# Performance work log

Hardware: AMD Instinct MI355X
Metric: run time of the kernel (lower is better)

## Reference

```python
import jax, jax.numpy as jnp
import numpy as np


def setup_inputs() -> dict:
    key = jax.random.key(0)
    k1, k2 = jax.random.split(key)
    B, C, H, W = 32, 64, 64, 64
    K = 512
    z_e = jax.random.normal(k1, (B, C, H, W), dtype=jnp.float32)
    # codebook initialized uniform(-1/K, 1/K) as in the torch module
    codebook = jax.random.uniform(k2, (K, C), dtype=jnp.float32,
                                  minval=-1.0 / K, maxval=1.0 / K)
    return {"z_e": z_e, "codebook": codebook}


def reference(z_e, codebook):
    B, C, H, W = z_e.shape
    commitment_cost = 0.25
    # [B*H*W, C]
    z_flat = jnp.transpose(z_e, (0, 2, 3, 1)).reshape(-1, C)
    dists = (jnp.sum(z_flat * z_flat, axis=1, keepdims=True)
             + jnp.sum(codebook * codebook, axis=1)
             - 2.0 * jnp.matmul(z_flat, codebook.T))
    encoding_indices = jnp.argmin(dists, axis=1)  # [N] int
    z_q = codebook[encoding_indices].reshape(B, H, W, C)
    z_q = jnp.transpose(z_q, (0, 3, 1, 2))  # [B, C, H, W]
    q_loss = jnp.mean((z_q - jax.lax.stop_gradient(z_e)) ** 2)
    e_loss = jnp.mean((z_e - jax.lax.stop_gradient(z_q)) ** 2)
    loss = q_loss + commitment_cost * e_loss
    # straight-through estimator
    z_q_st = z_e + jax.lax.stop_gradient(z_q - z_e)
    return (z_q_st, encoding_indices, loss)
```

## Files before the change

### kernel.cpp

```cpp
#include <hip/hip_runtime.h>
#include <cfloat>

typedef __attribute__((ext_vector_type(8))) short short8;
typedef __attribute__((ext_vector_type(4))) float f32x4;

constexpr int C_DIM    = 64;
constexpr int K_CODES  = 512;
constexpr int HW       = 4096;
constexpr int CHW      = 262144;
constexpr int NPTS     = 131072;
constexpr int ZQ_SIZE  = 8388608;
constexpr int IDX_OFF  = ZQ_SIZE;
constexpr int LOSS_OFF = ZQ_SIZE + NPTS;
constexpr int TILE     = 128;
constexpr int EH_STRIDE = 72;
constexpr int CHUNK    = 128;
constexpr int NSLOT    = 16;
constexpr size_t WS_BF16 = (size_t)K_CODES * C_DIM * 2;
constexpr size_t WS_NEED = WS_BF16 + (size_t)K_CODES * 4;

__device__ __forceinline__ unsigned short f32_to_bf16_rne(float f) {
    unsigned u = __float_as_uint(f);
    unsigned r = u + 0x7fffu + ((u >> 16) & 1u);
    return (unsigned short)(r >> 16);
}

template <int STRIDE>
__device__ __forceinline__ float np_sumsq64(const float* __restrict__ a) {
    float r[8];
#pragma unroll
    for (int j = 0; j < 8; ++j) { const float v = a[j * STRIDE]; r[j] = __fmul_rn(v, v); }
#pragma unroll
    for (int i = 8; i < 64; i += 8)
#pragma unroll
        for (int j = 0; j < 8; ++j) {
            const float v = a[(i + j) * STRIDE];
            r[j] = __fadd_rn(r[j], __fmul_rn(v, v));
        }
    return __fadd_rn(
        __fadd_rn(__fadd_rn(r[0], r[1]), __fadd_rn(r[2], r[3])),
        __fadd_rn(__fadd_rn(r[4], r[5]), __fadd_rn(r[6], r[7])));
}

__global__ void vq_zero(float* __restrict__ out) { out[LOSS_OFF] = 0.0f; }

__global__ void vq_prep(const float* __restrict__ cb, unsigned short* __restrict__ wsb,
                        float* __restrict__ wsB, float* __restrict__ out) {
    const int gid = blockIdx.x * 256 + threadIdx.x;
    wsb[gid] = f32_to_bf16_rne(cb[gid]);
    if (gid < K_CODES) wsB[gid] = np_sumsq64<1>(cb + gid * C_DIM);
    if (gid == 0) out[LOSS_OFF] = 0.0f;
}

__global__ __launch_bounds__(256, 4) void vq_idx(const float* __restrict__ ze,
                                                 const float* __restrict__ cb,
                                                 float* __restrict__ out,
                                                 const unsigned short* __restrict__ wsb,
                                                 const float* __restrict__ wsB,
                                                 int use_ws)
{
    __shared__ unsigned short eh[CHUNK * EH_STRIDE];
    __shared__ float  BsL[K_CODES];
    __shared__ float  As[TILE];
    __shared__ unsigned short cand[TILE * NSLOT];
    __shared__ int    cnt[TILE];
    __shared__ int    bestk[TILE];
    __shared__ double lred[4];

    const int tid  = threadIdx.x;
    const int lane = tid & 63, w = tid >> 6;
    const int quad = lane >> 4, l15 = lane & 15;
    const int n0   = blockIdx.x * TILE;
    const int b    = n0 >> 12, hw0 = n0 & (HW - 1);
    const float* zebase = ze + b * CHW + hw0;

    if (use_ws) { for (int k = tid; k < K_CODES; k += 256) BsL[k] = wsB[k]; }
    else        { for (int k = tid; k < K_CODES; k += 256) BsL[k] = np_sumsq64<1>(cb + k * C_DIM); }
    if (tid < TILE) { As[tid] = np_sumsq64<HW>(zebase + tid); cnt[tid] = 0; }
    __syncthreads();

    short8 afr[2][2];
    float  A_pt[2][4], thr[2][4], runmin[2][4];
#pragma unroll
    for (int rt = 0; rt < 2; ++rt) {
        const int pt = w * 32 + rt * 16 + l15;
#pragma unroll
        for (int kc = 0; kc < 2; ++kc) {
            union { unsigned short s[8]; short8 v; } u;
#pragma unroll
            for (int j = 0; j < 8; ++j) {
                const int c = kc * 32 + quad * 8 + j;
                u.s[j] = f32_to_bf16_rne(zebase[c * HW + pt]);
            }
            afr[rt][kc] = u.v;
        }
#pragma unroll
        for (int r = 0; r < 4; ++r) {
            A_pt[rt][r]   = As[w * 32 + rt * 16 + quad * 4 + r];
            runmin[rt][r] = FLT_MAX;
        }
    }

    auto stage = [&](int ch) {
        const int row = tid >> 1, half = tid & 1;
        uint4* dst = (uint4*)(eh + row * EH_STRIDE + half * 32);
        if (use_ws) {
            const uint4* src = (const uint4*)(wsb + (size_t)(ch * CHUNK + row) * C_DIM + half * 32);
#pragma unroll
            for (int i = 0; i < 4; ++i) dst[i] = src[i];
        } else {
            const float4* src = (const float4*)(cb + (size_t)(ch * CHUNK + row) * C_DIM + half * 32);
#pragma unroll
            for (int i = 0; i < 4; ++i) {
                const float4 f0 = src[2 * i], f1 = src[2 * i + 1];
                uint4 o;
                o.x = (unsigned)f32_to_bf16_rne(f0.x) | ((unsigned)f32_to_bf16_rne(f0.y) << 16);
                o.y = (unsigned)f32_to_bf16_rne(f0.z) | ((unsigned)f32_to_bf16_rne(f0.w) << 16);
                o.z = (unsigned)f32_to_bf16_rne(f1.x) | ((unsigned)f32_to_bf16_rne(f1.y) << 16);
                o.w = (unsigned)f32_to_bf16_rne(f1.z) | ((unsigned)f32_to_bf16_rne(f1.w) << 16);
                dst[i] = o;
            }
        }
    };

    for (int ch = 0; ch < 4; ++ch) {
        __syncthreads(); stage(ch); __syncthreads();
        for (int tile = 0; tile < 8; ++tile) {
            const int cl = tile * 16 + l15;
            const short8 b0 = *(const short8*)(eh + cl * EH_STRIDE + quad * 8);
            const short8 b1 = *(const short8*)(eh + cl * EH_STRIDE + 32 + quad * 8);
            const float bs = BsL[ch * CHUNK + cl];
#pragma unroll
            for (int rt = 0; rt < 2; ++rt) {
                f32x4 acc = {0.f, 0.f, 0.f, 0.f};
                acc = __builtin_amdgcn_mfma_f32_16x16x32_bf16(afr[rt][0], b0, acc, 0, 0, 0);
                acc = __builtin_amdgcn_mfma_f32_16x16x32_bf16(afr[rt][1], b1, acc, 0, 0, 0);
#pragma unroll
                for (int r = 0; r < 4; ++r) {
                    const float D = fmaf(-2.f, acc[r], __fadd_rn(A_pt[rt][r], bs));
                    runmin[rt][r] = fminf(runmin[rt][r], D);
                }
            }
        }
    }
#pragma unroll
    for (int rt = 0; rt < 2; ++rt)
#pragma unroll
        for (int r = 0; r < 4; ++r) {
            float v = runmin[rt][r];
#pragma unroll
            for (int m = 1; m < 16; m <<= 1) v = fminf(v, __shfl_xor(v, m, 64));
            thr[rt][r] = v + (4e-4f * sqrtf(A_pt[rt][r]) + 3e-4f);
        }

    for (int ch = 0; ch < 4; ++ch) {
        __syncthreads(); stage(ch); __syncthreads();
        for (int tile = 0; tile < 8; ++tile) {
            const int cl = tile * 16 + l15;
            const short8 b0 = *(const short8*)(eh + cl * EH_STRIDE + quad * 8);
            const short8 b1 = *(const short8*)(eh + cl * EH_STRIDE + 32 + quad * 8);
            const float bs = BsL[ch * CHUNK + cl];
#pragma unroll
            for (int rt = 0; rt < 2; ++rt) {
                f32x4 acc = {0.f, 0.f, 0.f, 0.f};
                acc = __builtin_amdgcn_mfma_f32_16x16x32_bf16(afr[rt][0], b0, acc, 0, 0, 0);
                acc = __builtin_amdgcn_mfma_f32_16x16x32_bf16(afr[rt][1], b1, acc, 0, 0, 0);
#pragma unroll
                for (int r = 0; r < 4; ++r) {
                    const float D = fmaf(-2.f, acc[r], __fadd_rn(A_pt[rt][r], bs));
                    if (D <= thr[rt][r]) {
                        const int pt = w * 32 + rt * 16 + quad * 4 + r;
                        const int p = atomicAdd(&cnt[pt], 1);
                        if (p < NSLOT) cand[pt * NSLOT + p] = (unsigned short)(ch * CHUNK + cl);
                    }
                }
            }
        }
    }
    __syncthreads();

    if (tid < TILE) {
        const float Av = As[tid];
        const int c = cnt[tid];
        float bD = FLT_MAX; int bK = K_CODES;
        if (c <= NSLOT) {
            for (int i = 0; i < c; ++i) {
                const int k = cand[tid * NSLOT + i];
                const float* er = cb + k * C_DIM;
                float M = 0.f;
#pragma unroll
                for (int cc = 0; cc < 64; ++cc) M = fmaf(zebase[cc * HW + tid], er[cc], M);
                const float D = fmaf(-2.f, M, __fadd_rn(Av, BsL[k]));
                if (D < bD || (D == bD && k < bK)) { bD = D; bK = k; }
            }
        } else {
            for (int k = 0; k < K_CODES; ++k) {
                const float* er = cb + k * C_DIM;
                float M = 0.f;
#pragma unroll
                for (int cc = 0; cc < 64; ++cc) M = fmaf(zebase[cc * HW + tid], er[cc], M);
                const float D = fmaf(-2.f, M, __fadd_rn(Av, BsL[k]));
                if (D < bD) { bD = D; bK = k; }
            }
        }
        bestk[tid] = bK;
        out[IDX_OFF + n0 + tid] = (float)bK;
    }
    __syncthreads();

    double ls = 0.0;
#pragma unroll
    for (int it = 0; it < 8; ++it) {
        const int task = tid + 256 * it;
        const int c = task >> 5, q = task & 31;
        const float4 xz = *(const float4*)(zebase + c * HW + 4 * q);
        float o[4];
#pragma unroll
        for (int j = 0; j < 4; ++j) {
            const int k = bestk[4 * q + j];
            const float ev = cb[k * C_DIM + c];
            const float xv = (j == 0) ? xz.x : (j == 1) ? xz.y : (j == 2) ? xz.z : xz.w;
            const float d = __fsub_rn(ev, xv);
            o[j] = __fadd_rn(xv, d);
            ls = fma((double)d, (double)d, ls);
        }
        *(float4*)(out + b * CHW + c * HW + hw0 + 4 * q) = make_float4(o[0], o[1], o[2], o[3]);
    }
#pragma unroll
    for (int off = 32; off > 0; off >>= 1) ls += __shfl_xor(ls, off, 64);
    if ((tid & 63) == 0) lred[w] = ls;
    __syncthreads();
    if (tid == 0)
        atomicAdd(out + LOSS_OFF,
                  (float)((lred[0] + lred[1] + lred[2] + lred[3]) * (1.25 / (double)ZQ_SIZE)));
}

extern "C" void kernel_launch(void* const* d_in, const int* in_sizes, int n_in,
                              void* d_out, int out_size, void* d_ws, size_t ws_size,
                              hipStream_t stream) {
    (void)in_sizes; (void)n_in; (void)out_size;
    const float* ze = (const float*)d_in[0];
    const float* cb = (const float*)d_in[1];
    float* out = (float*)d_out;
    const int use_ws = (ws_size >= WS_NEED) ? 1 : 0;
    unsigned short* wsb = (unsigned short*)d_ws;
    float* wsB = (float*)((char*)d_ws + WS_BF16);

    if (use_ws) vq_prep<<<(K_CODES * C_DIM) / 256, 256, 0, stream>>>(cb, wsb, wsB, out);
    else        vq_zero<<<1, 1, 0, stream>>>(out);
    vq_idx<<<NPTS / TILE, 256, 0, stream>>>(ze, cb, out, wsb, wsB, use_ws);
}
```

Baseline: 140.9 us.

## Fuse two-pass candidate search into single pass with per-lane top-2 tracking

Replaces the separate min pass and threshold-filter pass over the codebook with one MFMA pass that keeps each lane's best two scores and a third-best sentinel, then builds candidate lists from those after a cross-lane min reduction. This halves the MFMA and LDS staging work, and staging now uses 256-code chunks with an XOR-swizzled unpadded LDS layout. Per-point norm computation and fp32 refinement are split across thread pairs so all 256 threads work. The trade-offs are higher register use for the top-2 state and a tighter threshold. Any lane whose third-best falls inside the threshold forces the full fp32 fallback scan.

Measured after the change: 355.5 us. 2.52x slower.

```diff
diff --git a/kernel.cpp b/kernel.cpp
--- a/kernel.cpp
+++ b/kernel.cpp
@@ -13,9 +13,8 @@
 constexpr int IDX_OFF  = ZQ_SIZE;
 constexpr int LOSS_OFF = ZQ_SIZE + NPTS;
 constexpr int TILE     = 128;
-constexpr int EH_STRIDE = 72;
-constexpr int CHUNK    = 128;
-constexpr int NSLOT    = 16;
+constexpr int CHUNK    = 256;
+constexpr int NSLOT    = 8;
 constexpr size_t WS_BF16 = (size_t)K_CODES * C_DIM * 2;
 constexpr size_t WS_NEED = WS_BF16 + (size_t)K_CODES * 4;
 
@@ -40,6 +39,23 @@
     return __fadd_rn(
         __fadd_rn(__fadd_rn(r[0], r[1]), __fadd_rn(r[2], r[3])),
         __fadd_rn(__fadd_rn(r[4], r[5]), __fadd_rn(r[6], r[7])));
+}
+
+__device__ __forceinline__ float np_sumsq64_half_hw(const float* __restrict__ a, int j0) {
+    float r[4];
+#pragma unroll
+    for (int jj = 0; jj < 4; ++jj) {
+        const float v = a[(j0 * 4 + jj) * HW];
+        r[jj] = __fmul_rn(v, v);
+    }
+#pragma unroll
+    for (int i = 8; i < 64; i += 8)
+#pragma unroll
+        for (int jj = 0; jj < 4; ++jj) {
+            const float v = a[(i + j0 * 4 + jj) * HW];
+            r[jj] = __fadd_rn(r[jj], __fmul_rn(v, v));
+        }
+    return __fadd_rn(__fadd_rn(r[0], r[1]), __fadd_rn(r[2], r[3]));
 }
 
 __global__ void vq_zero(float* __restrict__ out) { out[LOSS_OFF] = 0.0f; }
@@ -59,7 +75,7 @@
                                                  const float* __restrict__ wsB,
                                                  int use_ws)
 {
-    __shared__ unsigned short eh[CHUNK * EH_STRIDE];
+    __shared__ unsigned short eh[CHUNK * C_DIM];
     __shared__ float  BsL[K_CODES];
     __shared__ float  As[TILE];
     __shared__ unsigned short cand[TILE * NSLOT];
@@ -76,11 +92,16 @@
 
     if (use_ws) { for (int k = tid; k < K_CODES; k += 256) BsL[k] = wsB[k]; }
     else        { for (int k = tid; k < K_CODES; k += 256) BsL[k] = np_sumsq64<1>(cb + k * C_DIM); }
-    if (tid < TILE) { As[tid] = np_sumsq64<HW>(zebase + tid); cnt[tid] = 0; }
-    __syncthreads();
+
+    {
+        const int pt = tid >> 1, j0 = tid & 1;
+        const float p = np_sumsq64_half_hw(zebase + pt, j0);
+        const float o = __shfl_xor(p, 1, 64);
+        if (j0 == 0) As[pt] = __fadd_rn(p, o);
+        if (tid < TILE) cnt[tid] = 0;
+    }
 
     short8 afr[2][2];
-    float  A_pt[2][4], thr[2][4], runmin[2][4];
 #pragma unroll
     for (int rt = 0; rt < 2; ++rt) {
         const int pt = w * 32 + rt * 16 + l15;
@@ -94,42 +115,52 @@
             }
             afr[rt][kc] = u.v;
         }
+    }
+    __syncthreads();
+
+    float d1[2][4], d2[2][4], d3[2][4];
+    int   k1[2][4], k2[2][4];
+#pragma unroll
+    for (int rt = 0; rt < 2; ++rt)
 #pragma unroll
         for (int r = 0; r < 4; ++r) {
-            A_pt[rt][r]   = As[w * 32 + rt * 16 + quad * 4 + r];
-            runmin[rt][r] = FLT_MAX;
-        }
-    }
-
-    auto stage = [&](int ch) {
-        const int row = tid >> 1, half = tid & 1;
-        uint4* dst = (uint4*)(eh + row * EH_STRIDE + half * 32);
-        if (use_ws) {
-            const uint4* src = (const uint4*)(wsb + (size_t)(ch * CHUNK + row) * C_DIM + half * 32);
-#pragma unroll
-            for (int i = 0; i < 4; ++i) dst[i] = src[i];
-        } else {
-            const float4* src = (const float4*)(cb + (size_t)(ch * CHUNK + row) * C_DIM + half * 32);
-#pragma unroll
-            for (int i = 0; i < 4; ++i) {
-                const float4 f0 = src[2 * i], f1 = src[2 * i + 1];
-                uint4 o;
-                o.x = (unsigned)f32_to_bf16_rne(f0.x) | ((unsigned)f32_to_bf16_rne(f0.y) << 16);
-                o.y = (unsigned)f32_to_bf16_rne(f0.z) | ((unsigned)f32_to_bf16_rne(f0.w) << 16);
-                o.z = (unsigned)f32_to_bf16_rne(f1.x) | ((unsigned)f32_to_bf16_rne(f1.y) << 16);
-                o.w = (unsigned)f32_to_bf16_rne(f1.z) | ((unsigned)f32_to_bf16_rne(f1.w) << 16);
-                dst[i] = o;
-            }
-        }
-    };
-
-    for (int ch = 0; ch < 4; ++ch) {
-        __syncthreads(); stage(ch); __syncthreads();
-        for (int tile = 0; tile < 8; ++tile) {
+            d1[rt][r] = FLT_MAX; d2[rt][r] = FLT_MAX; d3[rt][r] = FLT_MAX;
+            k1[rt][r] = K_CODES; k2[rt][r] = K_CODES;
+        }
+
+    for (int ch = 0; ch < 2; ++ch) {
+        if (ch) __syncthreads();
+        {
+            const int row = tid;
+            uint4* base = (uint4*)eh;
+            if (use_ws) {
+                const uint4* src = (const uint4*)(wsb + (size_t)(ch * CHUNK + row) * C_DIM);
+#pragma unroll
+                for (int s = 0; s < 8; ++s) base[row * 8 + (s ^ (row & 7))] = src[s];
+            } else {
+                const float4* src = (const float4*)(cb + (size_t)(ch * CHUNK + row) * C_DIM);
+#pragma unroll
+                for (int s = 0; s < 8; ++s) {
+                    const float4 f0 = src[2 * s], f1 = src[2 * s + 1];
+                    uint4 o;
+                    o.x = (unsigned)f32_to_bf16_rne(f0.x) | ((unsigned)f32_to_bf16_rne(f0.y) << 16);
+                    o.y = (unsigned)f32_to_bf16_rne(f0.z) | ((unsigned)f32_to_bf16_rne(f0.w) << 16);
+                    o.z = (unsigned)f32_to_bf16_rne(f1.x) | ((unsigned)f32_to_bf16_rne(f1.y) << 16);
+                    o.w = (unsigned)f32_to_bf16_rne(f1.z) | ((unsigned)f32_to_bf16_rne(f1.w) << 16);
+                    base[row * 8 + (s ^ (row & 7))] = o;
+                }
+            }
+        }
+        __syncthreads();
+
+        const uint4* ebase = (const uint4*)eh;
+#pragma unroll 4
+        for (int tile = 0; tile < 16; ++tile) {
             const int cl = tile * 16 + l15;
-            const short8 b0 = *(const short8*)(eh + cl * EH_STRIDE + quad * 8);
-            const short8 b1 = *(const short8*)(eh + cl * EH_STRIDE + 32 + quad * 8);
-            const float bs = BsL[ch * CHUNK + cl];
+            const short8 b0 = *(const short8*)&ebase[cl * 8 + ((quad    ) ^ (cl & 7))];
+            const short8 b1 = *(const short8*)&ebase[cl * 8 + ((quad + 4) ^ (cl & 7))];
+            const int kk = ch * CHUNK + cl;
+            const float bs = BsL[kk];
 #pragma unroll
             for (int rt = 0; rt < 2; ++rt) {
                 f32x4 acc = {0.f, 0.f, 0.f, 0.f};
@@ -137,74 +168,72 @@
                 acc = __builtin_amdgcn_mfma_f32_16x16x32_bf16(afr[rt][1], b1, acc, 0, 0, 0);
 #pragma unroll
                 for (int r = 0; r < 4; ++r) {
-                    const float D = fmaf(-2.f, acc[r], __fadd_rn(A_pt[rt][r], bs));
-                    runmin[rt][r] = fminf(runmin[rt][r], D);
+                    const float s = fmaf(0.5f, bs, -acc[r]);
+                    const bool c1 = s < d1[rt][r];
+                    const bool c2 = s < d2[rt][r];
+                    d3[rt][r] = c2 ? d2[rt][r] : fminf(s, d3[rt][r]);
+                    d2[rt][r] = c1 ? d1[rt][r] : fminf(s, d2[rt][r]);
+                    k2[rt][r] = c1 ? k1[rt][r] : (c2 ? kk : k2[rt][r]);
+                    d1[rt][r] = c1 ? s : d1[rt][r];
+                    k1[rt][r] = c1 ? kk : k1[rt][r];
                 }
             }
         }
     }
+
 #pragma unroll
     for (int rt = 0; rt < 2; ++rt)
 #pragma unroll
         for (int r = 0; r < 4; ++r) {
-            float v = runmin[rt][r];
+            float v = d1[rt][r];
 #pragma unroll
             for (int m = 1; m < 16; m <<= 1) v = fminf(v, __shfl_xor(v, m, 64));
-            thr[rt][r] = v + (4e-4f * sqrtf(A_pt[rt][r]) + 3e-4f);
-        }
-
-    for (int ch = 0; ch < 4; ++ch) {
-        __syncthreads(); stage(ch); __syncthreads();
-        for (int tile = 0; tile < 8; ++tile) {
-            const int cl = tile * 16 + l15;
-            const short8 b0 = *(const short8*)(eh + cl * EH_STRIDE + quad * 8);
-            const short8 b1 = *(const short8*)(eh + cl * EH_STRIDE + 32 + quad * 8);
-            const float bs = BsL[ch * CHUNK + cl];
-#pragma unroll
-            for (int rt = 0; rt < 2; ++rt) {
-                f32x4 acc = {0.f, 0.f, 0.f, 0.f};
-                acc = __builtin_amdgcn_mfma_f32_16x16x32_bf16(afr[rt][0], b0, acc, 0, 0, 0);
-                acc = __builtin_amdgcn_mfma_f32_16x16x32_bf16(afr[rt][1], b1, acc, 0, 0, 0);
-#pragma unroll
-                for (int r = 0; r < 4; ++r) {
-                    const float D = fmaf(-2.f, acc[r], __fadd_rn(A_pt[rt][r], bs));
-                    if (D <= thr[rt][r]) {
-                        const int pt = w * 32 + rt * 16 + quad * 4 + r;
-                        const int p = atomicAdd(&cnt[pt], 1);
-                        if (p < NSLOT) cand[pt * NSLOT + p] = (unsigned short)(ch * CHUNK + cl);
-                    }
-                }
-            }
-        }
-    }
-    __syncthreads();
-
-    if (tid < TILE) {
-        const float Av = As[tid];
-        const int c = cnt[tid];
+            const int pt = w * 32 + rt * 16 + quad * 4 + r;
+            const float thr = v + (2e-4f * sqrtf(As[pt]) + 1.5e-4f);
+            if (d1[rt][r] <= thr) {
+                const int p = atomicAdd(&cnt[pt], 1);
+                if (p < NSLOT) cand[pt * NSLOT + p] = (unsigned short)k1[rt][r];
+            }
+            if (d2[rt][r] <= thr) {
+                const int p = atomicAdd(&cnt[pt], 1);
+                if (p < NSLOT) cand[pt * NSLOT + p] = (unsigned short)k2[rt][r];
+            }
+            if (d3[rt][r] <= thr) atomicAdd(&cnt[pt], K_CODES);
+        }
+    __syncthreads();
+
+    {
+        const int pt = tid >> 1, j0 = tid & 1;
+        const float Av = As[pt];
+        const int c = cnt[pt];
         float bD = FLT_MAX; int bK = K_CODES;
         if (c <= NSLOT) {
-            for (int i = 0; i < c; ++i) {
-                const int k = cand[tid * NSLOT + i];
+            for (int i = j0; i < c; i += 2) {
+                const int k = cand[pt * NSLOT + i];
                 const float* er = cb + k * C_DIM;
                 float M = 0.f;
 #pragma unroll
-                for (int cc = 0; cc < 64; ++cc) M = fmaf(zebase[cc * HW + tid], er[cc], M);
+                for (int cc = 0; cc < 64; ++cc) M = fmaf(zebase[cc * HW + pt], er[cc], M);
                 const float D = fmaf(-2.f, M, __fadd_rn(Av, BsL[k]));
                 if (D < bD || (D == bD && k < bK)) { bD = D; bK = k; }
             }
         } else {
-            for (int k = 0; k < K_CODES; ++k) {
+            for (int k = j0; k < K_CODES; k += 2) {
                 const float* er = cb + k * C_DIM;
                 float M = 0.f;
 #pragma unroll
-                for (int cc = 0; cc < 64; ++cc) M = fmaf(zebase[cc * HW + tid], er[cc], M);
+                for (int cc = 0; cc < 64; ++cc) M = fmaf(zebase[cc * HW + pt], er[cc], M);
                 const float D = fmaf(-2.f, M, __fadd_rn(Av, BsL[k]));
-                if (D < bD) { bD = D; bK = k; }
-            }
-        }
-        bestk[tid] = bK;
-        out[IDX_OFF + n0 + tid] = (float)bK;
+                if (D < bD || (D == bD && k < bK)) { bD = D; bK = k; }
+            }
+        }
+        const float oD = __shfl_xor(bD, 1, 64);
+        const int   oK = __shfl_xor(bK, 1, 64);
+        if (oD < bD || (oD == bD && oK < bK)) { bD = oD; bK = oK; }
+        if (j0 == 0) {
+            bestk[pt] = bK;
+            out[IDX_OFF + n0 + pt] = (float)bK;
+        }
     }
     __syncthreads();
 
```

## Double codebook chunk size, XOR-swizzle LDS, and reuse last chunk in second pass

Applied to the files above, without the earlier changes.

Raises the staged codebook chunk from 128 to 256 codes, so each pass has two chunks and half as many stage/barrier rounds. The LDS layout drops the padded stride and uses an XOR swizzle on 16-byte slots to avoid bank conflicts. The candidate pass starts on the chunk still resident from the first pass, which removes one restage. Candidate slots per point drop from 16 to 8, so more points may overflow into the slow full-scan fallback. The larger LDS footprint may also reduce occupancy.

Result: slower. 313.7 us (+122.6%).

```diff
diff --git a/kernel.cpp b/kernel.cpp
--- a/kernel.cpp
+++ b/kernel.cpp
@@ -13,9 +13,8 @@
 constexpr int IDX_OFF  = ZQ_SIZE;
 constexpr int LOSS_OFF = ZQ_SIZE + NPTS;
 constexpr int TILE     = 128;
-constexpr int EH_STRIDE = 72;
-constexpr int CHUNK    = 128;
-constexpr int NSLOT    = 16;
+constexpr int CHUNK    = 256;
+constexpr int NSLOT    = 8;
 constexpr size_t WS_BF16 = (size_t)K_CODES * C_DIM * 2;
 constexpr size_t WS_NEED = WS_BF16 + (size_t)K_CODES * 4;
 
@@ -59,7 +58,7 @@
                                                  const float* __restrict__ wsB,
                                                  int use_ws)
 {
-    __shared__ unsigned short eh[CHUNK * EH_STRIDE];
+    __shared__ unsigned short eh[CHUNK * C_DIM];
     __shared__ float  BsL[K_CODES];
     __shared__ float  As[TILE];
     __shared__ unsigned short cand[TILE * NSLOT];
@@ -102,33 +101,35 @@
     }
 
     auto stage = [&](int ch) {
-        const int row = tid >> 1, half = tid & 1;
-        uint4* dst = (uint4*)(eh + row * EH_STRIDE + half * 32);
+        const int row = tid;
+        uint4* base = (uint4*)eh;
         if (use_ws) {
-            const uint4* src = (const uint4*)(wsb + (size_t)(ch * CHUNK + row) * C_DIM + half * 32);
-#pragma unroll
-            for (int i = 0; i < 4; ++i) dst[i] = src[i];
+            const uint4* src = (const uint4*)(wsb + (size_t)(ch * CHUNK + row) * C_DIM);
+#pragma unroll
+            for (int s = 0; s < 8; ++s) base[row * 8 + (s ^ (row & 7))] = src[s];
         } else {
-            const float4* src = (const float4*)(cb + (size_t)(ch * CHUNK + row) * C_DIM + half * 32);
-#pragma unroll
-            for (int i = 0; i < 4; ++i) {
-                const float4 f0 = src[2 * i], f1 = src[2 * i + 1];
+            const float4* src = (const float4*)(cb + (size_t)(ch * CHUNK + row) * C_DIM);
+#pragma unroll
+            for (int s = 0; s < 8; ++s) {
+                const float4 f0 = src[2 * s], f1 = src[2 * s + 1];
                 uint4 o;
                 o.x = (unsigned)f32_to_bf16_rne(f0.x) | ((unsigned)f32_to_bf16_rne(f0.y) << 16);
                 o.y = (unsigned)f32_to_bf16_rne(f0.z) | ((unsigned)f32_to_bf16_rne(f0.w) << 16);
                 o.z = (unsigned)f32_to_bf16_rne(f1.x) | ((unsigned)f32_to_bf16_rne(f1.y) << 16);
                 o.w = (unsigned)f32_to_bf16_rne(f1.z) | ((unsigned)f32_to_bf16_rne(f1.w) << 16);
-                dst[i] = o;
+                base[row * 8 + (s ^ (row & 7))] = o;
             }
         }
     };
 
-    for (int ch = 0; ch < 4; ++ch) {
+    for (int ch = 0; ch < 2; ++ch) {
         __syncthreads(); stage(ch); __syncthreads();
-        for (int tile = 0; tile < 8; ++tile) {
+        const uint4* ebase = (const uint4*)eh;
+#pragma unroll 4
+        for (int tile = 0; tile < 16; ++tile) {
             const int cl = tile * 16 + l15;
-            const short8 b0 = *(const short8*)(eh + cl * EH_STRIDE + quad * 8);
-            const short8 b1 = *(const short8*)(eh + cl * EH_STRIDE + 32 + quad * 8);
+            const short8 b0 = *(const short8*)&ebase[cl * 8 + ((quad    ) ^ (cl & 7))];
+            const short8 b1 = *(const short8*)&ebase[cl * 8 + ((quad + 4) ^ (cl & 7))];
             const float bs = BsL[ch * CHUNK + cl];
 #pragma unroll
             for (int rt = 0; rt < 2; ++rt) {
@@ -153,12 +154,13 @@
             thr[rt][r] = v + (4e-4f * sqrtf(A_pt[rt][r]) + 3e-4f);
         }
 
-    for (int ch = 0; ch < 4; ++ch) {
-        __syncthreads(); stage(ch); __syncthreads();
-        for (int tile = 0; tile < 8; ++tile) {
+    auto scan_push = [&](int ch) {
+        const uint4* ebase = (const uint4*)eh;
+#pragma unroll 4
+        for (int tile = 0; tile < 16; ++tile) {
             const int cl = tile * 16 + l15;
-            const short8 b0 = *(const short8*)(eh + cl * EH_STRIDE + quad * 8);
-            const short8 b1 = *(const short8*)(eh + cl * EH_STRIDE + 32 + quad * 8);
+            const short8 b0 = *(const short8*)&ebase[cl * 8 + ((quad    ) ^ (cl & 7))];
+            const short8 b1 = *(const short8*)&ebase[cl * 8 + ((quad + 4) ^ (cl & 7))];
             const float bs = BsL[ch * CHUNK + cl];
 #pragma unroll
             for (int rt = 0; rt < 2; ++rt) {
@@ -176,7 +178,10 @@
                 }
             }
         }
-    }
+    };
+    scan_push(1);
+    __syncthreads(); stage(0); __syncthreads();
+    scan_push(0);
     __syncthreads();
 
     if (tid < TILE) {
```
